# Performance work log

Hardware: AMD Instinct MI355X
Metric: run time of the kernel (lower is better)

The kernel has to match this reference:

```python
import jax, jax.numpy as jnp
import numpy as np

N_NODES = 100000
N_EDGES = 3200000
D_FEAT = 256
K_MAX = 5
NEG_SLOPE = 0.2


def _segment_softmax(e, seg, n):
    m = jax.ops.segment_max(e, seg, num_segments=n)
    ex = jnp.exp(e - m[seg])
    s = jax.ops.segment_sum(ex, seg, num_segments=n)
    return ex / (s[seg] + 1e-16)


def setup_inputs() -> dict:
    key = jax.random.key(0)
    ks = jax.random.split(key, 8)
    x = jax.random.normal(ks[0], (N_NODES, D_FEAT), dtype=jnp.float32)
    pos = jax.random.normal(ks[1], (N_NODES, 3), dtype=jnp.float32)
    w_l = jax.random.normal(ks[2], (D_FEAT, 1), dtype=jnp.float32) / np.sqrt(D_FEAT)
    w_r = jax.random.normal(ks[3], (D_FEAT, 1), dtype=jnp.float32) / np.sqrt(D_FEAT)
    w_e = jax.random.normal(ks[4], (3, 1), dtype=jnp.float32)
    att = jax.random.normal(ks[5], (1,), dtype=jnp.float32)
    bias = jnp.zeros((1,), dtype=jnp.float32)
    edge_index = jax.random.randint(ks[6], (2, N_EDGES), 0, N_NODES, dtype=jnp.int64)
    return {"x": x, "pos": pos, "w_l": w_l, "w_r": w_r, "w_e": w_e,
            "att": att, "bias": bias, "edge_index": edge_index}


def reference(x, pos, w_l, w_r, w_e, att, bias, edge_index):
    src, dst = edge_index[0], edge_index[1]
    n = x.shape[0]
    # GATv2Conv (heads=1, out_channels=1) scoring
    xl = x @ w_l                                  # [N,1] source transform
    xr = x @ w_r                                  # [N,1] target transform
    ea = (pos[dst] - pos[src]) @ w_e              # [E,1] edge-attr transform
    msg = xl[src] + xr[dst] + ea                  # [E,1]
    e = (jax.nn.leaky_relu(msg, NEG_SLOPE) * att).sum(-1)  # [E]
    alpha = _segment_softmax(e, dst, n)           # attention over incoming edges
    out = jax.ops.segment_sum(alpha[:, None] * xl[src], dst, num_segments=n) + bias
    logits = out[:, 0]                            # [N]
    score = jax.nn.softmax(logits)                # global node score

    # select highest-score node, grow k-hop neighborhood (<= k_max hops)
    node_id = jnp.argmax(jax.lax.stop_gradient(score))
    reach = jnp.zeros((n,), dtype=bool).at[node_id].set(True)
    for _ in range(K_MAX):
        frontier = jax.ops.segment_max(reach[src].astype(jnp.int32), dst,
                                       num_segments=n) > 0
        reach = reach | frontier
    reach = jax.lax.stop_gradient(reach)

    # pool_val = max over neighborhood features (Neighborhood.pool_val)
    pooled = jnp.max(jnp.where(reach[:, None], x, -jnp.inf), axis=0)  # [D]
    return jnp.concatenate([score, pooled])
```

## Files before the change

### kernel.cpp

```cpp
#include <hip/hip_runtime.h>

#define D_FEAT 256
#define NEG_SLOPE 0.2f
#define MAXBINS 512
#define SENT 0xFFFFFFFFu

__device__ __forceinline__ unsigned fmap(float f) {
    unsigned u = __float_as_uint(f);
    return (u & 0x80000000u) ? ~u : (u | 0x80000000u);
}
__device__ __forceinline__ float funmap(unsigned u) {
    return __uint_as_float((u & 0x80000000u) ? (u ^ 0x80000000u) : ~u);
}


__global__ void k_init(float2* NS, unsigned* stampW, int nW, unsigned* pooled_u,
                       unsigned* sc, unsigned* gHist, int n) {
    int i = blockIdx.x * blockDim.x + threadIdx.x;
    if (i < n) NS[i] = make_float2(0.f, 0.f);
    if (i < nW) stampW[i] = 0xFFFFFFFFu;
    if (i < D_FEAT) pooled_u[i] = 0u;
    if (i < MAXBINS) gHist[i] = 0u;
    if (i == 0) {
        sc[0] = 0u; ((float*)sc)[1] = 0.f; sc[2] = 0xFFFFFFFFu;
        sc[4] = 0u; sc[5] = 0u; sc[6] = 0xFFFFFFFFu; sc[7] = 0xFFFFFFFFu;
    }
}

__global__ void k_dots(const float* __restrict__ x, const float* __restrict__ w_l,
                       const float* __restrict__ w_r, float* __restrict__ xl,
                       float* __restrict__ xr, int n) {
    int wave = (int)((blockIdx.x * blockDim.x + threadIdx.x) >> 6);
    int lane = threadIdx.x & 63;
    if (wave >= n) return;
    const float4* xv = (const float4*)(x + (size_t)wave * D_FEAT);
    float4 v = xv[lane];
    float4 a = ((const float4*)w_l)[lane];
    float4 b = ((const float4*)w_r)[lane];
    float sl = v.x * a.x + v.y * a.y + v.z * a.z + v.w * a.w;
    float sr = v.x * b.x + v.y * b.y + v.z * b.z + v.w * b.w;
    #pragma unroll
    for (int o = 32; o; o >>= 1) { sl += __shfl_xor(sl, o); sr += __shfl_xor(sr, o); }
    if (lane == 0) { xl[wave] = sl; xr[wave] = sr; }
}

__global__ void k_ab(const float* __restrict__ xl, const float* __restrict__ xr,
                     const float* __restrict__ pos, const float* __restrict__ w_e,
                     float2* __restrict__ sA, float* __restrict__ B,
                     unsigned* sc, int n) {
    int i = blockIdx.x * blockDim.x + threadIdx.x;
    float amax, amin, bmax, bmin;
    if (i < n) {
        float p = pos[3 * i] * w_e[0] + pos[3 * i + 1] * w_e[1] + pos[3 * i + 2] * w_e[2];
        float xli = xl[i];
        float a = xli - p;
        float b = xr[i] + p;
        sA[i] = make_float2(a, xli);
        B[i] = b;
        amax = amin = a; bmax = bmin = b;
    } else {
        amax = bmax = -INFINITY; amin = bmin = INFINITY;
    }
    #pragma unroll
    for (int o = 32; o; o >>= 1) {
        amax = fmaxf(amax, __shfl_xor(amax, o));
        bmax = fmaxf(bmax, __shfl_xor(bmax, o));
        amin = fminf(amin, __shfl_xor(amin, o));
        bmin = fminf(bmin, __shfl_xor(bmin, o));
    }
    __shared__ float s4[4][4];
    int w = threadIdx.x >> 6, l = threadIdx.x & 63;
    if (l == 0) { s4[w][0] = amax; s4[w][1] = bmax; s4[w][2] = amin; s4[w][3] = bmin; }
    __syncthreads();
    if (threadIdx.x == 0) {
        float AM = s4[0][0], BM = s4[0][1], Am = s4[0][2], Bm = s4[0][3];
        #pragma unroll
        for (int k = 1; k < 4; ++k) {
            AM = fmaxf(AM, s4[k][0]); BM = fmaxf(BM, s4[k][1]);
            Am = fminf(Am, s4[k][2]); Bm = fminf(Bm, s4[k][3]);
        }
        atomicMax(&sc[4], fmap(AM)); atomicMax(&sc[5], fmap(BM));
        atomicMin(&sc[6], fmap(Am)); atomicMin(&sc[7], fmap(Bm));
    }
}


__global__ void k_hist(const int4* __restrict__ dst4, int E4, int nbins,
                       unsigned* __restrict__ gHist) {
    __shared__ unsigned h[MAXBINS];
    for (int b = threadIdx.x; b < nbins; b += blockDim.x) h[b] = 0u;
    __syncthreads();
    int stride = gridDim.x * blockDim.x;
    for (int i = blockIdx.x * blockDim.x + threadIdx.x; i < E4; i += stride) {
        int4 d = dst4[i];
        atomicAdd(&h[d.x >> 8], 1u);
        atomicAdd(&h[d.y >> 8], 1u);
        atomicAdd(&h[d.z >> 8], 1u);
        atomicAdd(&h[d.w >> 8], 1u);
    }
    __syncthreads();
    for (int b = threadIdx.x; b < nbins; b += blockDim.x)
        if (h[b]) atomicAdd(&gHist[b], h[b]);
}

__global__ void k_scan(const unsigned* __restrict__ gHist, unsigned* __restrict__ gBase,
                       unsigned* __restrict__ gCursor, int nbins, int nBlk,
                       unsigned* sc, const float* __restrict__ att) {
    int lane = threadIdx.x;
    if (lane == 0) {
        float at = att[0];
        float z = (at >= 0.f) ? (funmap(sc[4]) + funmap(sc[5]))
                              : (funmap(sc[6]) + funmap(sc[7]));
        float lz = (z >= 0.f) ? z : NEG_SLOPE * z;
        ((float*)sc)[3] = lz * at;
    }
    unsigned padw = 15u * (unsigned)nBlk;
    unsigned carry = 0;
    for (int b0 = 0; b0 < nbins; b0 += 64) {
        int b = b0 + lane;
        unsigned v = (b < nbins) ? ((gHist[b] + padw + 15u) & ~15u) : 0u;
        unsigned inc = v;
        #pragma unroll
        for (int o = 1; o < 64; o <<= 1) {
            unsigned t = __shfl_up(inc, o);
            if (lane >= o) inc += t;
        }
        unsigned excl = inc - v + carry;
        if (b < nbins) { gBase[b] = excl; gCursor[b] = excl; }
        carry += __shfl(inc, 63);
    }
}

__global__ void k_scatter(const int4* __restrict__ src4, const int4* __restrict__ dst4,
                          unsigned* __restrict__ gCursor, unsigned* __restrict__ recs,
                          int E4, int nbins) {
    __shared__ unsigned h[MAXBINS];
    __shared__ unsigned base[MAXBINS];
    for (int b = threadIdx.x; b < nbins; b += 512) h[b] = 0u;
    __syncthreads();
    int b4 = blockIdx.x * 2048;
    #pragma unroll
    for (int g = 0; g < 4; ++g) {
        int idx = b4 + g * 512 + threadIdx.x;
        if (idx < E4) {
            int4 d = dst4[idx];
            atomicAdd(&h[d.x >> 8], 1u);
            atomicAdd(&h[d.y >> 8], 1u);
            atomicAdd(&h[d.z >> 8], 1u);
            atomicAdd(&h[d.w >> 8], 1u);
        }
    }
    __syncthreads();
    for (int b = threadIdx.x; b < nbins; b += 512) {
        unsigned c = h[b];
        h[b] = 0u;
        base[b] = c ? atomicAdd(&gCursor[b], (c + 15u) & ~15u) : 0u;
    }
    __syncthreads();
    #pragma unroll
    for (int g = 0; g < 4; ++g) {
        int idx = b4 + g * 512 + threadIdx.x;
        if (idx < E4) {
            int4 sv = src4[idx];
            int4 dv = dst4[idx];
            int ss[4] = { sv.x, sv.y, sv.z, sv.w };
            int dd[4] = { dv.x, dv.y, dv.z, dv.w };
            #pragma unroll
            for (int j = 0; j < 4; ++j) {
                int d_ = dd[j];
                int bin = d_ >> 8;
                unsigned off = atomicAdd(&h[bin], 1u);
                recs[base[bin] + off] = (unsigned)ss[j] | ((unsigned)(d_ & 255) << 17);
            }
        }
    }
    __syncthreads();
    for (int b = threadIdx.x; b < nbins; b += 512) {
        unsigned c = h[b];
        unsigned pc = (c + 15u) & ~15u;
        for (unsigned k = c; k < pc; ++k) recs[base[b] + k] = SENT;
    }
}

__global__ void k_binsum(const unsigned* __restrict__ recs, const unsigned* __restrict__ gBase,
                         const unsigned* __restrict__ gCursor,
                         const float2* __restrict__ sA, const float* __restrict__ B,
                         const float* __restrict__ att, const float* __restrict__ bias,
                         float* __restrict__ logits, unsigned* sc, int n) {
    __shared__ float accx[256];
    __shared__ float accy[256];
    __shared__ float Bb[256];
    int b = blockIdx.x;
    int tid = threadIdx.x;
    int node0 = b << 8;
    accx[tid] = 0.f; accy[tid] = 0.f;
    Bb[tid] = (node0 + tid < n) ? B[node0 + tid] : 0.f;
    __syncthreads();
    const float at = att[0];
    const float M = ((const float*)sc)[3];
    unsigned s0 = gBase[b], s1 = gCursor[b];
    for (unsigned i = s0 + tid; i < s1; i += 256u) {
        unsigned w = recs[i];
        if (w == SENT) continue;
        int src = (int)(w & 0x1FFFFu);
        int loc = (int)(w >> 17);
        float2 sa = sA[src];
        float msg = sa.x + Bb[loc];
        float lr = (msg >= 0.f) ? msg : NEG_SLOPE * msg;
        float e = expf(lr * at - M);
        atomicAdd(&accx[loc], e);
        atomicAdd(&accy[loc], e * sa.y);
    }
    __syncthreads();
    int node = node0 + tid;
    float lg = -INFINITY;
    if (node < n) {
        lg = accy[tid] / (accx[tid] + 1e-38f) + bias[0];
        logits[node] = lg;
    }
    unsigned mu = fmap(lg);
    #pragma unroll
    for (int o = 32; o; o >>= 1) { unsigned t = __shfl_xor(mu, o); mu = (t > mu) ? t : mu; }
    __shared__ unsigned wm[4];
    int w_ = tid >> 6, l = tid & 63;
    if (l == 0) wm[w_] = mu;
    __syncthreads();
    if (tid == 0) {
        unsigned m = wm[0];
        #pragma unroll
        for (int k = 1; k < 4; ++k) m = (wm[k] > m) ? wm[k] : m;
        atomicMax(&sc[0], m);
    }
}


__global__ void k_edge_sum(const int* __restrict__ src, const int* __restrict__ dst,
                           const float2* __restrict__ sA, const float* __restrict__ B,
                           const float* __restrict__ att, const unsigned* __restrict__ sc,
                           float2* NS, int E) {
    int i = blockIdx.x * blockDim.x + threadIdx.x;
    if (i >= E) return;
    int s = src[i], d = dst[i];
    float2 sa = sA[s];
    float msg = sa.x + B[d];
    float lr = (msg >= 0.f) ? msg : NEG_SLOPE * msg;
    float ex = expf(lr * att[0] - ((const float*)sc)[3]);
    atomicAdd(&NS[d].x, ex);
    atomicAdd(&NS[d].y, ex * sa.y);
}

__global__ void k_logits(const float2* __restrict__ NS, const float* __restrict__ bias,
                         float* __restrict__ logits, unsigned* sc, int n) {
    int i = blockIdx.x * blockDim.x + threadIdx.x;
    unsigned mu = 0u;
    if (i < n) {
        float2 ns = NS[i];
        float lg = ns.y / (ns.x + 1e-38f) + bias[0];
        logits[i] = lg;
        mu = fmap(lg);
    }
    #pragma unroll
    for (int o = 32; o; o >>= 1) { unsigned t = __shfl_xor(mu, o); mu = (t > mu) ? t : mu; }
    if ((threadIdx.x & 63) == 0) atomicMax(&sc[0], mu);
}


__global__ void k_sumarg(const float* __restrict__ logits, unsigned* sc, int n) {
    int i = blockIdx.x * blockDim.x + threadIdx.x;
    unsigned gmax_u = sc[0];
    float gmax = funmap(gmax_u);
    float ex = 0.f;
    if (i < n) {
        float lg = logits[i];
        ex = expf(lg - gmax);
        if (fmap(lg) == gmax_u) atomicMin(&sc[2], (unsigned)i);
    }
    #pragma unroll
    for (int o = 32; o; o >>= 1) ex += __shfl_xor(ex, o);
    if ((threadIdx.x & 63) == 0) atomicAdd((float*)&sc[1], ex);
}

__global__ void k_score(const float* __restrict__ logits, const unsigned* __restrict__ sc,
                        float* __restrict__ out, unsigned char* stamp, int n) {
    int i = blockIdx.x * blockDim.x + threadIdx.x;
    if (i >= n) return;
    float gmax = funmap(sc[0]);
    float gsum = ((const float*)sc)[1];
    out[i] = expf(logits[i] - gmax) / gsum;
    if (i == (int)sc[2]) stamp[i] = 0;
}

__global__ void k_bfs_stamp(const int4* __restrict__ src4, const int4* __restrict__ dst4,
                            unsigned char* __restrict__ stamp, int E4, int t) {
    int i = blockIdx.x * blockDim.x + threadIdx.x;
    if (i >= E4) return;
    int4 s = src4[i];
    unsigned char th = (unsigned char)t;
    bool h0 = stamp[s.x] < th;
    bool h1 = stamp[s.y] < th;
    bool h2 = stamp[s.z] < th;
    bool h3 = stamp[s.w] < th;
    if (!(h0 | h1 | h2 | h3)) return;
    int4 d = dst4[i];
    if (h0 && stamp[d.x] > th) stamp[d.x] = th;
    if (h1 && stamp[d.y] > th) stamp[d.y] = th;
    if (h2 && stamp[d.z] > th) stamp[d.z] = th;
    if (h3 && stamp[d.w] > th) stamp[d.w] = th;
}

__global__ void k_pool1(const float* __restrict__ x, const unsigned char* __restrict__ stamp,
                        float4* __restrict__ partial, int n) {
    int sub = threadIdx.x >> 6;
    int lane = threadIdx.x & 63;
    float4 m = make_float4(-INFINITY, -INFINITY, -INFINITY, -INFINITY);
    int stride = gridDim.x * 4;
    for (int node = blockIdx.x * 4 + sub; node < n; node += stride) {
        if (stamp[node] != 0xFF) {
            float4 v = ((const float4*)(x + (size_t)node * D_FEAT))[lane];
            m.x = fmaxf(m.x, v.x); m.y = fmaxf(m.y, v.y);
            m.z = fmaxf(m.z, v.z); m.w = fmaxf(m.w, v.w);
        }
    }
    __shared__ float4 red[256];
    red[threadIdx.x] = m;
    __syncthreads();
    if (sub == 0) {
        float4 a = red[lane], b = red[64 + lane], c = red[128 + lane], d = red[192 + lane];
        a.x = fmaxf(fmaxf(a.x, b.x), fmaxf(c.x, d.x));
        a.y = fmaxf(fmaxf(a.y, b.y), fmaxf(c.y, d.y));
        a.z = fmaxf(fmaxf(a.z, b.z), fmaxf(c.z, d.z));
        a.w = fmaxf(fmaxf(a.w, b.w), fmaxf(c.w, d.w));
        partial[(size_t)blockIdx.x * 64 + lane] = a;
    }
}

__global__ void k_pool2(const float4* __restrict__ partial, int nblk1, unsigned* pooled_u) {
    int sub = threadIdx.x >> 6;
    int lane = threadIdx.x & 63;
    int chunk = (nblk1 + gridDim.x - 1) / gridDim.x;
    int b0 = blockIdx.x * chunk;
    int b1 = min(b0 + chunk, nblk1);
    float4 m = make_float4(-INFINITY, -INFINITY, -INFINITY, -INFINITY);
    for (int b = b0 + sub; b < b1; b += 4) {
        float4 v = partial[(size_t)b * 64 + lane];
        m.x = fmaxf(m.x, v.x); m.y = fmaxf(m.y, v.y);
        m.z = fmaxf(m.z, v.z); m.w = fmaxf(m.w, v.w);
    }
    __shared__ float4 red[256];
    red[threadIdx.x] = m;
    __syncthreads();
    if (sub == 0) {
        float4 a = red[lane], b = red[64 + lane], c = red[128 + lane], d = red[192 + lane];
        a.x = fmaxf(fmaxf(a.x, b.x), fmaxf(c.x, d.x));
        a.y = fmaxf(fmaxf(a.y, b.y), fmaxf(c.y, d.y));
        a.z = fmaxf(fmaxf(a.z, b.z), fmaxf(c.z, d.z));
        a.w = fmaxf(fmaxf(a.w, b.w), fmaxf(c.w, d.w));
        atomicMax(&pooled_u[lane * 4 + 0], fmap(a.x));
        atomicMax(&pooled_u[lane * 4 + 1], fmap(a.y));
        atomicMax(&pooled_u[lane * 4 + 2], fmap(a.z));
        atomicMax(&pooled_u[lane * 4 + 3], fmap(a.w));
    }
}

__global__ void k_poolwrite(const unsigned* __restrict__ pooled_u, float* __restrict__ out, int n) {
    int t = threadIdx.x;
    out[n + t] = funmap(pooled_u[t]);
}

extern "C" void kernel_launch(void* const* d_in, const int* in_sizes, int n_in,
                              void* d_out, int out_size, void* d_ws, size_t ws_size,
                              hipStream_t stream) {
    const float* x    = (const float*)d_in[0];
    const float* pos  = (const float*)d_in[1];
    const float* w_l  = (const float*)d_in[2];
    const float* w_r  = (const float*)d_in[3];
    const float* w_e  = (const float*)d_in[4];
    const float* att  = (const float*)d_in[5];
    const float* bias = (const float*)d_in[6];
    const int*   ei   = (const int*)d_in[7];

    const int n = in_sizes[0] / D_FEAT;
    const int E = in_sizes[7] / 2;
    const int* src = ei;
    const int* dst = ei + E;
    const int nbins = (n + 255) >> 8;
    const int nW = (n + 3) / 4;
    const int nBlkScat = (E + 8191) / 8192;

    float* f0 = (float*)d_ws;
    size_t o = 0;
    float*    xl       = f0 + o; o += (size_t)n;
    float*    xr       = f0 + o; o += (size_t)n;
    float2*   sA       = (float2*)(f0 + o); o += 2 * (size_t)n;
    float*    B        = f0 + o; o += (size_t)n;
    float*    logits   = f0 + o; o += (size_t)n;
    o = (o + 3) & ~(size_t)3;
    float2*   NS       = (float2*)(f0 + o); o += 2 * (size_t)n;
    float4*   partial  = (float4*)NS;
    unsigned* stampW   = (unsigned*)(f0 + o); o += (size_t)nW;
    unsigned char* stamp = (unsigned char*)stampW;
    unsigned* pooled_u = (unsigned*)(f0 + o); o += 256;
    unsigned* sc       = (unsigned*)(f0 + o); o += 64;
    unsigned* gHist    = (unsigned*)(f0 + o); o += MAXBINS;
    unsigned* gBase    = (unsigned*)(f0 + o); o += MAXBINS;
    unsigned* gCursor  = (unsigned*)(f0 + o); o += MAXBINS;
    o = (o + 15) & ~(size_t)15;
    unsigned* recs     = (unsigned*)(f0 + o);

    int nblk1 = (int)((2 * (size_t)n) / 256);
    if (nblk1 > 768) nblk1 = 768;
    if (nblk1 < 1) nblk1 = 1;

    size_t capWords = (size_t)E + (size_t)nbins * (15u * (size_t)nBlkScat + 16u);
    size_t need_bytes = (o + capWords) * sizeof(float);
    const bool sorted_ok = (ws_size >= need_bytes) && (nbins <= MAXBINS) &&
                           (E % 4 == 0) && (n <= (1 << 17));

    float* out = (float*)d_out;

    const int Bk = 256;
    const int gN  = (n + Bk - 1) / Bk;
    const int gE  = (E + Bk - 1) / Bk;
    const int gD  = (n + 3) / 4;
    const int E4  = E / 4;
    const int gE4 = (E4 + Bk - 1) / Bk;

    k_init<<<gN, Bk, 0, stream>>>(NS, stampW, nW, pooled_u, sc, gHist, n);
    k_dots<<<gD, Bk, 0, stream>>>(x, w_l, w_r, xl, xr, n);
    k_ab<<<gN, Bk, 0, stream>>>(xl, xr, pos, w_e, sA, B, sc, n);

    if (sorted_ok) {
        k_hist<<<512, Bk, 0, stream>>>((const int4*)dst, E4, nbins, gHist);
        k_scan<<<1, 64, 0, stream>>>(gHist, gBase, gCursor, nbins, nBlkScat, sc, att);
        k_scatter<<<nBlkScat, 512, 0, stream>>>((const int4*)src, (const int4*)dst,
                                                gCursor, recs, E4, nbins);
        k_binsum<<<nbins, Bk, 0, stream>>>(recs, gBase, gCursor, sA, B, att, bias,
                                           logits, sc, n);
    } else {
        k_scan<<<1, 64, 0, stream>>>(gHist, gBase, gCursor, 0, 0, sc, att);
        k_edge_sum<<<gE, Bk, 0, stream>>>(src, dst, sA, B, att, sc, NS, E);
        k_logits<<<gN, Bk, 0, stream>>>(NS, bias, logits, sc, n);
    }

    k_sumarg<<<gN, Bk, 0, stream>>>(logits, sc, n);
    k_score<<<gN, Bk, 0, stream>>>(logits, sc, out, stamp, n);

    for (int t = 1; t <= 5; ++t) {
        k_bfs_stamp<<<gE4, Bk, 0, stream>>>((const int4*)src, (const int4*)dst, stamp, E4, t);
    }

    k_pool1<<<nblk1, Bk, 0, stream>>>(x, stamp, partial, n);
    k_pool2<<<16, Bk, 0, stream>>>(partial, nblk1, pooled_u);
    k_poolwrite<<<1, Bk, 0, stream>>>(pooled_u, out, n);
}
```

Measured before the change: 280.9 us.

## Fuse preprocessing with histogram, reuse dst-sorted records for BFS, trim launches

Merges the init, dot-product, A/B and histogram kernels into one launch that writes per-block partials, reduced by a single scan kernel, so global atomics and a memset are no longer needed. The BFS hops now walk the dst-bucketed record array built for the softmax pass instead of rescanning the raw edge list, and each block exits early when all of its nodes are already stamped. The scatter block size doubles, binsum reads records as uint4, and pooling finishes with a single reduction kernel that writes the output directly. The cost is a more complex fused kernel and BFS that stays serialized per bin block.

After: 328.5 us. 1.17x slower.

```diff
diff --git a/kernel.cpp b/kernel.cpp
--- a/kernel.cpp
+++ b/kernel.cpp
@@ -3,6 +3,7 @@
 #define D_FEAT 256
 #define NEG_SLOPE 0.2f
 #define MAXBINS 512
+#define HISTB 64
 #define SENT 0xFFFFFFFFu
 
 __device__ __forceinline__ unsigned fmap(float f) {
@@ -14,13 +15,357 @@
 }
 
 
+__global__ void k_pre(const float* __restrict__ x, const float* __restrict__ w_l,
+                      const float* __restrict__ w_r, const float* __restrict__ pos,
+                      const float* __restrict__ w_e,
+                      float2* __restrict__ sA, float* __restrict__ Bv,
+                      float4* __restrict__ gABpart, unsigned* __restrict__ stampW,
+                      unsigned* __restrict__ gHistPart,
+                      const int4* __restrict__ dst4, int E4, int nbins,
+                      int n, int nW, int gD) {
+    int blk = blockIdx.x;
+    int tid = threadIdx.x;
+    if (blk < gD) {
+        int gid = blk * 256 + tid;
+        if (gid < nW) stampW[gid] = 0xFFFFFFFFu;
+        int w = tid >> 6, lane = tid & 63;
+        int node = blk * 4 + w;
+        __shared__ float s4[4][4];
+        if (node < n) {
+            const float4* xv = (const float4*)(x + (size_t)node * D_FEAT);
+            float4 v = xv[lane];
+            float4 al = ((const float4*)w_l)[lane];
+            float4 bl = ((const float4*)w_r)[lane];
+            float sl = v.x * al.x + v.y * al.y + v.z * al.z + v.w * al.w;
+            float sr = v.x * bl.x + v.y * bl.y + v.z * bl.z + v.w * bl.w;
+            #pragma unroll
+            for (int o = 32; o; o >>= 1) { sl += __shfl_xor(sl, o); sr += __shfl_xor(sr, o); }
+            if (lane == 0) {
+                float p = pos[3 * node] * w_e[0] + pos[3 * node + 1] * w_e[1]
+                        + pos[3 * node + 2] * w_e[2];
+                float a = sl - p;
+                float b = sr + p;
+                sA[node] = make_float2(a, sl);
+                Bv[node] = b;
+                s4[w][0] = a; s4[w][1] = b; s4[w][2] = a; s4[w][3] = b;
+            }
+        } else if (lane == 0) {
+            s4[w][0] = -INFINITY; s4[w][1] = -INFINITY;
+            s4[w][2] = INFINITY;  s4[w][3] = INFINITY;
+        }
+        __syncthreads();
+        if (tid == 0) {
+            float AM = s4[0][0], BM = s4[0][1], Am = s4[0][2], Bm = s4[0][3];
+            #pragma unroll
+            for (int k = 1; k < 4; ++k) {
+                AM = fmaxf(AM, s4[k][0]); BM = fmaxf(BM, s4[k][1]);
+                Am = fminf(Am, s4[k][2]); Bm = fminf(Bm, s4[k][3]);
+            }
+            gABpart[blk] = make_float4(AM, BM, Am, Bm);
+        }
+    } else {
+        int hb = blk - gD;
+        __shared__ unsigned h[MAXBINS];
+        for (int b = tid; b < nbins; b += 256) h[b] = 0u;
+        __syncthreads();
+        int stride = HISTB * 256;
+        for (int i = hb * 256 + tid; i < E4; i += stride) {
+            int4 d = dst4[i];
+            atomicAdd(&h[d.x >> 8], 1u);
+            atomicAdd(&h[d.y >> 8], 1u);
+            atomicAdd(&h[d.z >> 8], 1u);
+            atomicAdd(&h[d.w >> 8], 1u);
+        }
+        __syncthreads();
+        for (int b = tid; b < nbins; b += 256) gHistPart[hb * MAXBINS + b] = h[b];
+    }
+}
+
+__global__ void k_scan2(const float4* __restrict__ gABpart, int nAB,
+                        const unsigned* __restrict__ gHistPart,
+                        unsigned* __restrict__ gBase, unsigned* __restrict__ gCursor,
+                        int nbins, int nBlk, unsigned* sc, const float* __restrict__ att) {
+    int tid = threadIdx.x;
+    float AM = -INFINITY, BM = -INFINITY, Am = INFINITY, Bm = INFINITY;
+    for (int i = tid; i < nAB; i += 256) {
+        float4 v = gABpart[i];
+        AM = fmaxf(AM, v.x); BM = fmaxf(BM, v.y);
+        Am = fminf(Am, v.z); Bm = fminf(Bm, v.w);
+    }
+    #pragma unroll
+    for (int o = 32; o; o >>= 1) {
+        AM = fmaxf(AM, __shfl_xor(AM, o)); BM = fmaxf(BM, __shfl_xor(BM, o));
+        Am = fminf(Am, __shfl_xor(Am, o)); Bm = fminf(Bm, __shfl_xor(Bm, o));
+    }
+    __shared__ float s4[4][4];
+    int w = tid >> 6, lane = tid & 63;
+    if (lane == 0) { s4[w][0] = AM; s4[w][1] = BM; s4[w][2] = Am; s4[w][3] = Bm; }
+    __syncthreads();
+    if (tid == 0) {
+        float am = s4[0][0], bm = s4[0][1], an = s4[0][2], bn = s4[0][3];
+        #pragma unroll
+        for (int k = 1; k < 4; ++k) {
+            am = fmaxf(am, s4[k][0]); bm = fmaxf(bm, s4[k][1]);
+            an = fminf(an, s4[k][2]); bn = fminf(bn, s4[k][3]);
+        }
+        float at = att[0];
+        float z = (at >= 0.f) ? (am + bm) : (an + bn);
+        float lz = (z >= 0.f) ? z : NEG_SLOPE * z;
+        ((float*)sc)[3] = lz * at;
+        sc[0] = 0u; ((float*)sc)[1] = 0.f; sc[2] = 0xFFFFFFFFu;
+    }
+    __shared__ unsigned hs[MAXBINS];
+    for (int b = tid; b < nbins; b += 256) {
+        unsigned s = 0;
+        for (int p = 0; p < HISTB; ++p) s += gHistPart[p * MAXBINS + b];
+        hs[b] = s;
+    }
+    __syncthreads();
+    if (tid < 64) {
+        unsigned padw = 15u * (unsigned)nBlk;
+        unsigned carry = 0;
+        for (int b0 = 0; b0 < nbins; b0 += 64) {
+            int b = b0 + tid;
+            unsigned v = (b < nbins) ? ((hs[b] + padw + 15u) & ~15u) : 0u;
+            unsigned inc = v;
+            #pragma unroll
+            for (int o = 1; o < 64; o <<= 1) {
+                unsigned t = __shfl_up(inc, o);
+                if (tid >= o) inc += t;
+            }
+            unsigned excl = inc - v + carry;
+            if (b < nbins) { gBase[b] = excl; gCursor[b] = excl; }
+            carry += __shfl(inc, 63);
+        }
+    }
+}
+
+__global__ void k_scatter(const int4* __restrict__ src4, const int4* __restrict__ dst4,
+                          unsigned* __restrict__ gCursor, unsigned* __restrict__ recs,
+                          int E4, int nbins) {
+    __shared__ unsigned h[MAXBINS];
+    __shared__ unsigned base[MAXBINS];
+    for (int b = threadIdx.x; b < nbins; b += 512) h[b] = 0u;
+    __syncthreads();
+    int b4 = blockIdx.x * 4096;
+    #pragma unroll
+    for (int g = 0; g < 8; ++g) {
+        int idx = b4 + g * 512 + threadIdx.x;
+        if (idx < E4) {
+            int4 d = dst4[idx];
+            atomicAdd(&h[d.x >> 8], 1u);
+            atomicAdd(&h[d.y >> 8], 1u);
+            atomicAdd(&h[d.z >> 8], 1u);
+            atomicAdd(&h[d.w >> 8], 1u);
+        }
+    }
+    __syncthreads();
+    for (int b = threadIdx.x; b < nbins; b += 512) {
+        unsigned c = h[b];
+        h[b] = 0u;
+        base[b] = c ? atomicAdd(&gCursor[b], (c + 15u) & ~15u) : 0u;
+    }
+    __syncthreads();
+    #pragma unroll
+    for (int g = 0; g < 8; ++g) {
+        int idx = b4 + g * 512 + threadIdx.x;
+        if (idx < E4) {
+            int4 sv = src4[idx];
+            int4 dv = dst4[idx];
+            int ss[4] = { sv.x, sv.y, sv.z, sv.w };
+            int dd[4] = { dv.x, dv.y, dv.z, dv.w };
+            #pragma unroll
+            for (int j = 0; j < 4; ++j) {
+                int d_ = dd[j];
+                int bin = d_ >> 8;
+                unsigned off = atomicAdd(&h[bin], 1u);
+                recs[base[bin] + off] = (unsigned)ss[j] | ((unsigned)(d_ & 255) << 17);
+            }
+        }
+    }
+    __syncthreads();
+    for (int b = threadIdx.x; b < nbins; b += 512) {
+        unsigned c = h[b];
+        unsigned pc = (c + 15u) & ~15u;
+        for (unsigned k = c; k < pc; ++k) recs[base[b] + k] = SENT;
+    }
+}
+
+__global__ void k_binsum(const uint4* __restrict__ recs4, const unsigned* __restrict__ gBase,
+                         const unsigned* __restrict__ gCursor,
+                         const float2* __restrict__ sA, const float* __restrict__ Bv,
+                         const float* __restrict__ att, const float* __restrict__ bias,
+                         float* __restrict__ logits, unsigned* sc, int n) {
+    __shared__ float accx[256];
+    __shared__ float accy[256];
+    __shared__ float Bb[256];
+    int b = blockIdx.x;
+    int tid = threadIdx.x;
+    int node0 = b << 8;
+    accx[tid] = 0.f; accy[tid] = 0.f;
+    Bb[tid] = (node0 + tid < n) ? Bv[node0 + tid] : 0.f;
+    __syncthreads();
+    const float at = att[0];
+    const float M = ((const float*)sc)[3];
+    unsigned q0 = gBase[b] >> 2, q1 = gCursor[b] >> 2;
+    for (unsigned i = q0 + tid; i < q1; i += 256u) {
+        uint4 r4 = recs4[i];
+        unsigned ws[4] = { r4.x, r4.y, r4.z, r4.w };
+        #pragma unroll
+        for (int j = 0; j < 4; ++j) {
+            unsigned wv = ws[j];
+            if (wv == SENT) continue;
+            int sidx = (int)(wv & 0x1FFFFu);
+            int loc  = (int)(wv >> 17);
+            float2 sa = sA[sidx];
+            float msg = sa.x + Bb[loc];
+            float lr = (msg >= 0.f) ? msg : NEG_SLOPE * msg;
+            float e = expf(lr * at - M);
+            atomicAdd(&accx[loc], e);
+            atomicAdd(&accy[loc], e * sa.y);
+        }
+    }
+    __syncthreads();
+    int node = node0 + tid;
+    float lg = -INFINITY;
+    if (node < n) {
+        lg = accy[tid] / (accx[tid] + 1e-38f) + bias[0];
+        logits[node] = lg;
+    }
+    unsigned mu = fmap(lg);
+    #pragma unroll
+    for (int o = 32; o; o >>= 1) { unsigned t = __shfl_xor(mu, o); mu = (t > mu) ? t : mu; }
+    __shared__ unsigned wm[4];
+    int w_ = tid >> 6, l = tid & 63;
+    if (l == 0) wm[w_] = mu;
+    __syncthreads();
+    if (tid == 0) {
+        unsigned m = wm[0];
+        #pragma unroll
+        for (int k = 1; k < 4; ++k) m = (wm[k] > m) ? wm[k] : m;
+        atomicMax(&sc[0], m);
+    }
+}
+
+
+__global__ void k_sumarg(const float* __restrict__ logits, unsigned* sc, int n) {
+    int i = blockIdx.x * blockDim.x + threadIdx.x;
+    unsigned gmax_u = sc[0];
+    float gmax = funmap(gmax_u);
+    float ex = 0.f;
+    if (i < n) {
+        float lg = logits[i];
+        ex = expf(lg - gmax);
+        if (fmap(lg) == gmax_u) atomicMin(&sc[2], (unsigned)i);
+    }
+    #pragma unroll
+    for (int o = 32; o; o >>= 1) ex += __shfl_xor(ex, o);
+    if ((threadIdx.x & 63) == 0) atomicAdd((float*)&sc[1], ex);
+}
+
+__global__ void k_score(const float* __restrict__ logits, const unsigned* __restrict__ sc,
+                        float* __restrict__ out, unsigned char* stamp, int n) {
+    int i = blockIdx.x * blockDim.x + threadIdx.x;
+    if (i >= n) return;
+    float gmax = funmap(sc[0]);
+    float gsum = ((const float*)sc)[1];
+    out[i] = expf(logits[i] - gmax) / gsum;
+    if (i == (int)sc[2]) stamp[i] = 0;
+}
+
+__global__ void k_bfs_rec(const uint4* __restrict__ recs4, const unsigned* __restrict__ gBase,
+                          const unsigned* __restrict__ gCursor,
+                          unsigned char* __restrict__ stamp, int n, int t) {
+    __shared__ unsigned char st[256];
+    __shared__ unsigned char mark[256];
+    __shared__ unsigned char wn[4];
+    int b = blockIdx.x;
+    int tid = threadIdx.x;
+    int node = (b << 8) + tid;
+    unsigned char th = (unsigned char)t;
+    unsigned char s = (node < n) ? stamp[node] : (unsigned char)0;
+    st[tid] = s; mark[tid] = 0;
+    unsigned long long ball = __ballot(s > th);
+    if ((tid & 63) == 0) wn[tid >> 6] = (ball != 0ull) ? 1 : 0;
+    __syncthreads();
+    if (!(wn[0] | wn[1] | wn[2] | wn[3])) return;
+    unsigned q0 = gBase[b] >> 2, q1 = gCursor[b] >> 2;
+    for (unsigned i = q0 + tid; i < q1; i += 256u) {
+        uint4 r4 = recs4[i];
+        unsigned ws[4] = { r4.x, r4.y, r4.z, r4.w };
+        #pragma unroll
+        for (int j = 0; j < 4; ++j) {
+            unsigned wv = ws[j];
+            if (wv == SENT) continue;
+            int loc = (int)(wv >> 17);
+            if (st[loc] > th) {
+                if (stamp[wv & 0x1FFFFu] < th) mark[loc] = 1;
+            }
+        }
+    }
+    __syncthreads();
+    if (mark[tid] && node < n && st[tid] > th) stamp[node] = th;
+}
+
+__global__ void k_pool1(const float* __restrict__ x, const unsigned char* __restrict__ stamp,
+                        float4* __restrict__ partial, int n) {
+    int sub = threadIdx.x >> 6;
+    int lane = threadIdx.x & 63;
+    float4 m = make_float4(-INFINITY, -INFINITY, -INFINITY, -INFINITY);
+    int stride = gridDim.x * 4;
+    for (int node = blockIdx.x * 4 + sub; node < n; node += stride) {
+        if (stamp[node] != 0xFF) {
+            float4 v = ((const float4*)(x + (size_t)node * D_FEAT))[lane];
+            m.x = fmaxf(m.x, v.x); m.y = fmaxf(m.y, v.y);
+            m.z = fmaxf(m.z, v.z); m.w = fmaxf(m.w, v.w);
+        }
+    }
+    __shared__ float4 red[256];
+    red[threadIdx.x] = m;
+    __syncthreads();
+    if (sub == 0) {
+        float4 a = red[lane], b = red[64 + lane], c = red[128 + lane], d = red[192 + lane];
+        a.x = fmaxf(fmaxf(a.x, b.x), fmaxf(c.x, d.x));
+        a.y = fmaxf(fmaxf(a.y, b.y), fmaxf(c.y, d.y));
+        a.z = fmaxf(fmaxf(a.z, b.z), fmaxf(c.z, d.z));
+        a.w = fmaxf(fmaxf(a.w, b.w), fmaxf(c.w, d.w));
+        partial[(size_t)blockIdx.x * 64 + lane] = a;
+    }
+}
+
+__global__ void k_pool2f(const float4* __restrict__ partial, int nblk1,
+                         float* __restrict__ out, int n) {
+    int sub = threadIdx.x >> 6;
+    int lane = threadIdx.x & 63;
+    float4 m = make_float4(-INFINITY, -INFINITY, -INFINITY, -INFINITY);
+    for (int r = sub; r < nblk1; r += 4) {
+        float4 v = partial[(size_t)r * 64 + lane];
+        m.x = fmaxf(m.x, v.x); m.y = fmaxf(m.y, v.y);
+        m.z = fmaxf(m.z, v.z); m.w = fmaxf(m.w, v.w);
+    }
+    __shared__ float4 red[256];
+    red[threadIdx.x] = m;
+    __syncthreads();
+    if (sub == 0) {
+        float4 a = red[lane], b = red[64 + lane], c = red[128 + lane], d = red[192 + lane];
+        a.x = fmaxf(fmaxf(a.x, b.x), fmaxf(c.x, d.x));
+        a.y = fmaxf(fmaxf(a.y, b.y), fmaxf(c.y, d.y));
+        a.z = fmaxf(fmaxf(a.z, b.z), fmaxf(c.z, d.z));
+        a.w = fmaxf(fmaxf(a.w, b.w), fmaxf(c.w, d.w));
+        out[n + 4 * lane + 0] = a.x;
+        out[n + 4 * lane + 1] = a.y;
+        out[n + 4 * lane + 2] = a.z;
+        out[n + 4 * lane + 3] = a.w;
+    }
+}
+
+
 __global__ void k_init(float2* NS, unsigned* stampW, int nW, unsigned* pooled_u,
-                       unsigned* sc, unsigned* gHist, int n) {
+                       unsigned* sc, int n) {
     int i = blockIdx.x * blockDim.x + threadIdx.x;
     if (i < n) NS[i] = make_float2(0.f, 0.f);
     if (i < nW) stampW[i] = 0xFFFFFFFFu;
     if (i < D_FEAT) pooled_u[i] = 0u;
-    if (i < MAXBINS) gHist[i] = 0u;
     if (i == 0) {
         sc[0] = 0u; ((float*)sc)[1] = 0.f; sc[2] = 0xFFFFFFFFu;
         sc[4] = 0u; sc[5] = 0u; sc[6] = 0xFFFFFFFFu; sc[7] = 0xFFFFFFFFu;
@@ -84,155 +429,16 @@
     }
 }
 
-
-__global__ void k_hist(const int4* __restrict__ dst4, int E4, int nbins,
-                       unsigned* __restrict__ gHist) {
-    __shared__ unsigned h[MAXBINS];
-    for (int b = threadIdx.x; b < nbins; b += blockDim.x) h[b] = 0u;
-    __syncthreads();
-    int stride = gridDim.x * blockDim.x;
-    for (int i = blockIdx.x * blockDim.x + threadIdx.x; i < E4; i += stride) {
-        int4 d = dst4[i];
-        atomicAdd(&h[d.x >> 8], 1u);
-        atomicAdd(&h[d.y >> 8], 1u);
-        atomicAdd(&h[d.z >> 8], 1u);
-        atomicAdd(&h[d.w >> 8], 1u);
-    }
-    __syncthreads();
-    for (int b = threadIdx.x; b < nbins; b += blockDim.x)
-        if (h[b]) atomicAdd(&gHist[b], h[b]);
-}
-
-__global__ void k_scan(const unsigned* __restrict__ gHist, unsigned* __restrict__ gBase,
-                       unsigned* __restrict__ gCursor, int nbins, int nBlk,
-                       unsigned* sc, const float* __restrict__ att) {
-    int lane = threadIdx.x;
-    if (lane == 0) {
+__global__ void k_scanM(unsigned* sc, const float* __restrict__ att) {
+    if (threadIdx.x == 0) {
         float at = att[0];
         float z = (at >= 0.f) ? (funmap(sc[4]) + funmap(sc[5]))
                               : (funmap(sc[6]) + funmap(sc[7]));
         float lz = (z >= 0.f) ? z : NEG_SLOPE * z;
         ((float*)sc)[3] = lz * at;
-    }
-    unsigned padw = 15u * (unsigned)nBlk;
-    unsigned carry = 0;
-    for (int b0 = 0; b0 < nbins; b0 += 64) {
-        int b = b0 + lane;
-        unsigned v = (b < nbins) ? ((gHist[b] + padw + 15u) & ~15u) : 0u;
-        unsigned inc = v;
-        #pragma unroll
-        for (int o = 1; o < 64; o <<= 1) {
-            unsigned t = __shfl_up(inc, o);
-            if (lane >= o) inc += t;
-        }
-        unsigned excl = inc - v + carry;
-        if (b < nbins) { gBase[b] = excl; gCursor[b] = excl; }
-        carry += __shfl(inc, 63);
-    }
-}
-
-__global__ void k_scatter(const int4* __restrict__ src4, const int4* __restrict__ dst4,
-                          unsigned* __restrict__ gCursor, unsigned* __restrict__ recs,
-                          int E4, int nbins) {
-    __shared__ unsigned h[MAXBINS];
-    __shared__ unsigned base[MAXBINS];
-    for (int b = threadIdx.x; b < nbins; b += 512) h[b] = 0u;
-    __syncthreads();
-    int b4 = blockIdx.x * 2048;
-    #pragma unroll
-    for (int g = 0; g < 4; ++g) {
-        int idx = b4 + g * 512 + threadIdx.x;
-        if (idx < E4) {
-            int4 d = dst4[idx];
-            atomicAdd(&h[d.x >> 8], 1u);
-            atomicAdd(&h[d.y >> 8], 1u);
-            atomicAdd(&h[d.z >> 8], 1u);
-            atomicAdd(&h[d.w >> 8], 1u);
-        }
-    }
-    __syncthreads();
-    for (int b = threadIdx.x; b < nbins; b += 512) {
-        unsigned c = h[b];
-        h[b] = 0u;
-        base[b] = c ? atomicAdd(&gCursor[b], (c + 15u) & ~15u) : 0u;
-    }
-    __syncthreads();
-    #pragma unroll
-    for (int g = 0; g < 4; ++g) {
-        int idx = b4 + g * 512 + threadIdx.x;
-        if (idx < E4) {
-            int4 sv = src4[idx];
-            int4 dv = dst4[idx];
-            int ss[4] = { sv.x, sv.y, sv.z, sv.w };
-            int dd[4] = { dv.x, dv.y, dv.z, dv.w };
-            #pragma unroll
-            for (int j = 0; j < 4; ++j) {
-                int d_ = dd[j];
-                int bin = d_ >> 8;
-                unsigned off = atomicAdd(&h[bin], 1u);
-                recs[base[bin] + off] = (unsigned)ss[j] | ((unsigned)(d_ & 255) << 17);
-            }
-        }
-    }
-    __syncthreads();
-    for (int b = threadIdx.x; b < nbins; b += 512) {
-        unsigned c = h[b];
-        unsigned pc = (c + 15u) & ~15u;
-        for (unsigned k = c; k < pc; ++k) recs[base[b] + k] = SENT;
-    }
-}
-
-__global__ void k_binsum(const unsigned* __restrict__ recs, const unsigned* __restrict__ gBase,
-                         const unsigned* __restrict__ gCursor,
-                         const float2* __restrict__ sA, const float* __restrict__ B,
-                         const float* __restrict__ att, const float* __restrict__ bias,
-                         float* __restrict__ logits, unsigned* sc, int n) {
-    __shared__ float accx[256];
-    __shared__ float accy[256];
-    __shared__ float Bb[256];
-    int b = blockIdx.x;
-    int tid = threadIdx.x;
-    int node0 = b << 8;
-    accx[tid] = 0.f; accy[tid] = 0.f;
-    Bb[tid] = (node0 + tid < n) ? B[node0 + tid] : 0.f;
-    __syncthreads();
-    const float at = att[0];
-    const float M = ((const float*)sc)[3];
-    unsigned s0 = gBase[b], s1 = gCursor[b];
-    for (unsigned i = s0 + tid; i < s1; i += 256u) {
-        unsigned w = recs[i];
-        if (w == SENT) continue;
-        int src = (int)(w & 0x1FFFFu);
-        int loc = (int)(w >> 17);
-        float2 sa = sA[src];
-        float msg = sa.x + Bb[loc];
-        float lr = (msg >= 0.f) ? msg : NEG_SLOPE * msg;
-        float e = expf(lr * at - M);
-        atomicAdd(&accx[loc], e);
-        atomicAdd(&accy[loc], e * sa.y);
-    }
-    __syncthreads();
-    int node = node0 + tid;
-    float lg = -INFINITY;
-    if (node < n) {
-        lg = accy[tid] / (accx[tid] + 1e-38f) + bias[0];
-        logits[node] = lg;
-    }
-    unsigned mu = fmap(lg);
-    #pragma unroll
-    for (int o = 32; o; o >>= 1) { unsigned t = __shfl_xor(mu, o); mu = (t > mu) ? t : mu; }
-    __shared__ unsigned wm[4];
-    int w_ = tid >> 6, l = tid & 63;
-    if (l == 0) wm[w_] = mu;
-    __syncthreads();
-    if (tid == 0) {
-        unsigned m = wm[0];
-        #pragma unroll
-        for (int k = 1; k < 4; ++k) m = (wm[k] > m) ? wm[k] : m;
-        atomicMax(&sc[0], m);
-    }
-}
-
+        sc[0] = 0u; ((float*)sc)[1] = 0.f; sc[2] = 0xFFFFFFFFu;
+    }
+}
 
 __global__ void k_edge_sum(const int* __restrict__ src, const int* __restrict__ dst,
                            const float2* __restrict__ sA, const float* __restrict__ B,
@@ -262,32 +468,6 @@
     #pragma unroll
     for (int o = 32; o; o >>= 1) { unsigned t = __shfl_xor(mu, o); mu = (t > mu) ? t : mu; }
     if ((threadIdx.x & 63) == 0) atomicMax(&sc[0], mu);
-}
-
-
-__global__ void k_sumarg(const float* __restrict__ logits, unsigned* sc, int n) {
-    int i = blockIdx.x * blockDim.x + threadIdx.x;
-    unsigned gmax_u = sc[0];
-    float gmax = funmap(gmax_u);
-    float ex = 0.f;
-    if (i < n) {
-        float lg = logits[i];
-        ex = expf(lg - gmax);
-        if (fmap(lg) == gmax_u) atomicMin(&sc[2], (unsigned)i);
-    }
-    #pragma unroll
-    for (int o = 32; o; o >>= 1) ex += __shfl_xor(ex, o);
-    if ((threadIdx.x & 63) == 0) atomicAdd((float*)&sc[1], ex);
-}
-
-__global__ void k_score(const float* __restrict__ logits, const unsigned* __restrict__ sc,
-                        float* __restrict__ out, unsigned char* stamp, int n) {
-    int i = blockIdx.x * blockDim.x + threadIdx.x;
-    if (i >= n) return;
-    float gmax = funmap(sc[0]);
-    float gsum = ((const float*)sc)[1];
-    out[i] = expf(logits[i] - gmax) / gsum;
-    if (i == (int)sc[2]) stamp[i] = 0;
 }
 
 __global__ void k_bfs_stamp(const int4* __restrict__ src4, const int4* __restrict__ dst4,
@@ -308,32 +488,6 @@
     if (h3 && stamp[d.w] > th) stamp[d.w] = th;
 }
 
-__global__ void k_pool1(const float* __restrict__ x, const unsigned char* __restrict__ stamp,
-                        float4* __restrict__ partial, int n) {
-    int sub = threadIdx.x >> 6;
-    int lane = threadIdx.x & 63;
-    float4 m = make_float4(-INFINITY, -INFINITY, -INFINITY, -INFINITY);
-    int stride = gridDim.x * 4;
-    for (int node = blockIdx.x * 4 + sub; node < n; node += stride) {
-        if (stamp[node] != 0xFF) {
-            float4 v = ((const float4*)(x + (size_t)node * D_FEAT))[lane];
-            m.x = fmaxf(m.x, v.x); m.y = fmaxf(m.y, v.y);
-            m.z = fmaxf(m.z, v.z); m.w = fmaxf(m.w, v.w);
-        }
-    }
-    __shared__ float4 red[256];
-    red[threadIdx.x] = m;
-    __syncthreads();
-    if (sub == 0) {
-        float4 a = red[lane], b = red[64 + lane], c = red[128 + lane], d = red[192 + lane];
-        a.x = fmaxf(fmaxf(a.x, b.x), fmaxf(c.x, d.x));
-        a.y = fmaxf(fmaxf(a.y, b.y), fmaxf(c.y, d.y));
-        a.z = fmaxf(fmaxf(a.z, b.z), fmaxf(c.z, d.z));
-        a.w = fmaxf(fmaxf(a.w, b.w), fmaxf(c.w, d.w));
-        partial[(size_t)blockIdx.x * 64 + lane] = a;
-    }
-}
-
 __global__ void k_pool2(const float4* __restrict__ partial, int nblk1, unsigned* pooled_u) {
     int sub = threadIdx.x >> 6;
     int lane = threadIdx.x & 63;
@@ -385,7 +539,13 @@
     const int* dst = ei + E;
     const int nbins = (n + 255) >> 8;
     const int nW = (n + 3) / 4;
-    const int nBlkScat = (E + 8191) / 8192;
+    const int nBlkScat = (E + 16383) / 16384;
+    const int Bk = 256;
+    const int gN  = (n + Bk - 1) / Bk;
+    const int gE  = (E + Bk - 1) / Bk;
+    const int gD  = (n + 3) / 4;
+    const int E4  = E / 4;
+    const int gE4 = (E4 + Bk - 1) / Bk;
 
     float* f0 = (float*)d_ws;
     size_t o = 0;
@@ -396,20 +556,19 @@
     float*    logits   = f0 + o; o += (size_t)n;
     o = (o + 3) & ~(size_t)3;
     float2*   NS       = (float2*)(f0 + o); o += 2 * (size_t)n;
-    float4*   partial  = (float4*)NS;
+    float4*   partialF = (float4*)NS;
     unsigned* stampW   = (unsigned*)(f0 + o); o += (size_t)nW;
     unsigned char* stamp = (unsigned char*)stampW;
     unsigned* pooled_u = (unsigned*)(f0 + o); o += 256;
     unsigned* sc       = (unsigned*)(f0 + o); o += 64;
-    unsigned* gHist    = (unsigned*)(f0 + o); o += MAXBINS;
     unsigned* gBase    = (unsigned*)(f0 + o); o += MAXBINS;
     unsigned* gCursor  = (unsigned*)(f0 + o); o += MAXBINS;
+    o = (o + 3) & ~(size_t)3;
+    float4*   gABpart  = (float4*)(f0 + o); o += 4 * (size_t)gD;
+    unsigned* gHistPart= (unsigned*)(f0 + o); o += (size_t)HISTB * MAXBINS;
     o = (o + 15) & ~(size_t)15;
     unsigned* recs     = (unsigned*)(f0 + o);
-
-    int nblk1 = (int)((2 * (size_t)n) / 256);
-    if (nblk1 > 768) nblk1 = 768;
-    if (nblk1 < 1) nblk1 = 1;
+    float4*   partialT = (float4*)recs;
 
     size_t capWords = (size_t)E + (size_t)nbins * (15u * (size_t)nBlkScat + 16u);
     size_t need_bytes = (o + capWords) * sizeof(float);
@@ -418,38 +577,42 @@
 
     float* out = (float*)d_out;
 
-    const int Bk = 256;
-    const int gN  = (n + Bk - 1) / Bk;
-    const int gE  = (E + Bk - 1) / Bk;
-    const int gD  = (n + 3) / 4;
-    const int E4  = E / 4;
-    const int gE4 = (E4 + Bk - 1) / Bk;
-
-    k_init<<<gN, Bk, 0, stream>>>(NS, stampW, nW, pooled_u, sc, gHist, n);
-    k_dots<<<gD, Bk, 0, stream>>>(x, w_l, w_r, xl, xr, n);
-    k_ab<<<gN, Bk, 0, stream>>>(xl, xr, pos, w_e, sA, B, sc, n);
-
     if (sorted_ok) {
-        k_hist<<<512, Bk, 0, stream>>>((const int4*)dst, E4, nbins, gHist);
-        k_scan<<<1, 64, 0, stream>>>(gHist, gBase, gCursor, nbins, nBlkScat, sc, att);
+        k_pre<<<gD + HISTB, Bk, 0, stream>>>(x, w_l, w_r, pos, w_e, sA, B, gABpart,
+                                             stampW, gHistPart, (const int4*)dst,
+                                             E4, nbins, n, nW, gD);
+        k_scan2<<<1, Bk, 0, stream>>>(gABpart, gD, gHistPart, gBase, gCursor,
+                                      nbins, nBlkScat, sc, att);
         k_scatter<<<nBlkScat, 512, 0, stream>>>((const int4*)src, (const int4*)dst,
                                                 gCursor, recs, E4, nbins);
-        k_binsum<<<nbins, Bk, 0, stream>>>(recs, gBase, gCursor, sA, B, att, bias,
-                                           logits, sc, n);
+        k_binsum<<<nbins, Bk, 0, stream>>>((const uint4*)recs, gBase, gCursor, sA, B,
+                                           att, bias, logits, sc, n);
+        k_sumarg<<<gN, Bk, 0, stream>>>(logits, sc, n);
+        k_score<<<gN, Bk, 0, stream>>>(logits, sc, out, stamp, n);
+        for (int t = 1; t <= 5; ++t) {
+            k_bfs_rec<<<nbins, Bk, 0, stream>>>((const uint4*)recs, gBase, gCursor,
+                                                stamp, n, t);
+        }
+        k_pool1<<<768, Bk, 0, stream>>>(x, stamp, partialT, n);
+        k_pool2f<<<1, Bk, 0, stream>>>(partialT, 768, out, n);
     } else {
-        k_scan<<<1, 64, 0, stream>>>(gHist, gBase, gCursor, 0, 0, sc, att);
+        k_init<<<gN, Bk, 0, stream>>>(NS, stampW, nW, pooled_u, sc, n);
+        k_dots<<<gD, Bk, 0, stream>>>(x, w_l, w_r, xl, xr, n);
+        k_ab<<<gN, Bk, 0, stream>>>(xl, xr, pos, w_e, sA, B, sc, n);
+        k_scanM<<<1, 64, 0, stream>>>(sc, att);
         k_edge_sum<<<gE, Bk, 0, stream>>>(src, dst, sA, B, att, sc, NS, E);
         k_logits<<<gN, Bk, 0, stream>>>(NS, bias, logits, sc, n);
-    }
-
-    k_sumarg<<<gN, Bk, 0, stream>>>(logits, sc, n);
-    k_score<<<gN, Bk, 0, stream>>>(logits, sc, out, stamp, n);
-
-    for (int t = 1; t <= 5; ++t) {
-        k_bfs_stamp<<<gE4, Bk, 0, stream>>>((const int4*)src, (const int4*)dst, stamp, E4, t);
-    }
-
-    k_pool1<<<nblk1, Bk, 0, stream>>>(x, stamp, partial, n);
-    k_pool2<<<16, Bk, 0, stream>>>(partial, nblk1, pooled_u);
-    k_poolwrite<<<1, Bk, 0, stream>>>(pooled_u, out, n);
-}
+        k_sumarg<<<gN, Bk, 0, stream>>>(logits, sc, n);
+        k_score<<<gN, Bk, 0, stream>>>(logits, sc, out, stamp, n);
+        for (int t = 1; t <= 5; ++t) {
+            k_bfs_stamp<<<gE4, Bk, 0, stream>>>((const int4*)src, (const int4*)dst,
+                                                stamp, E4, t);
+        }
+        int nblk1 = (int)((2 * (size_t)n) / 256);
+        if (nblk1 > 768) nblk1 = 768;
+        if (nblk1 < 1) nblk1 = 1;
+        k_pool1<<<nblk1, Bk, 0, stream>>>(x, stamp, partialF, n);
+        k_pool2<<<16, Bk, 0, stream>>>(partialF, nblk1, pooled_u);
+        k_poolwrite<<<1, Bk, 0, stream>>>(pooled_u, out, n);
+    }
+}
```
